# Kernel tuning notes

Measured on AMD Instinct MI355X. Metric: run time of the kernel, lower is better.

The kernel has to match this reference:

```python
import jax, jax.numpy as jnp
import numpy as np

B, T, D = 4, 2048, 1024


def setup_inputs() -> dict:
    key = jax.random.key(0)
    ks = jax.random.split(key, 14)
    s = 0.02
    return {
        "x": jax.random.normal(ks[0], (B, T, D), dtype=jnp.float32),
        "time_decay": jax.random.normal(ks[1], (D,), dtype=jnp.float32) * 0.1,
        "tm_k": jax.random.uniform(ks[2], (D,), dtype=jnp.float32),
        "tm_v": jax.random.uniform(ks[3], (D,), dtype=jnp.float32),
        "tm_r": jax.random.uniform(ks[4], (D,), dtype=jnp.float32),
        "Wk": jax.random.normal(ks[5], (D, D), dtype=jnp.float32) * s,
        "Wv": jax.random.normal(ks[6], (D, D), dtype=jnp.float32) * s,
        "Wr": jax.random.normal(ks[7], (D, D), dtype=jnp.float32) * s,
        "Wo": jax.random.normal(ks[8], (D, D), dtype=jnp.float32) * s,
        "cm_k": jax.random.uniform(ks[9], (D,), dtype=jnp.float32),
        "cm_r": jax.random.uniform(ks[10], (D,), dtype=jnp.float32),
        "Wck": jax.random.normal(ks[11], (D, 4 * D), dtype=jnp.float32) * s,
        "Wcv": jax.random.normal(ks[12], (4 * D, D), dtype=jnp.float32) * s,
        "Wcr": jax.random.normal(ks[13], (D, D), dtype=jnp.float32) * s,
    }


def _shift(x):
    # token shift: prepend zero state (initial last_x), drop last token
    return jnp.concatenate([jnp.zeros_like(x[:, :1]), x[:, :-1]], axis=1)


def reference(x, time_decay, tm_k, tm_v, tm_r, Wk, Wv, Wr, Wo,
              cm_k, cm_r, Wck, Wcv, Wcr):
    # ---- time mixing (WKV recurrence) ----
    shifted = _shift(x)
    xk = x * tm_k + shifted * (1.0 - tm_k)
    xv = x * tm_v + shifted * (1.0 - tm_v)
    xr = x * tm_r + shifted * (1.0 - tm_r)
    k = xk @ Wk            # (B,T,D)
    v = xv @ Wv
    r = jax.nn.sigmoid(xr @ Wr)
    ew = jnp.exp(-jnp.exp(time_decay))  # exp(w), w = -exp(time_decay)

    def step(carry, kv):
        num, den = carry
        kt, vt = kv
        ek = jnp.exp(kt)
        num = ew * num + ek * vt
        den = ew * den + ek
        return (num, den), num / (den + 1e-6)

    init = (jnp.zeros((B, D), x.dtype), jnp.zeros((B, D), x.dtype))
    _, wkv_t = jax.lax.scan(step, init, (jnp.swapaxes(k, 0, 1), jnp.swapaxes(v, 0, 1)))
    wkv = jnp.swapaxes(wkv_t, 0, 1)  # (B,T,D)
    x = x + (r * wkv) @ Wo

    # ---- channel mixing (gated FFN, squared ReLU) ----
    shifted2 = _shift(x)
    xk2 = x * cm_k + shifted2 * (1.0 - cm_k)
    xr2 = x * cm_r + shifted2 * (1.0 - cm_r)
    kh = jnp.square(jax.nn.relu(xk2 @ Wck))  # (B,T,4D)
    v2 = kh @ Wcv
    r2 = jax.nn.sigmoid(xr2 @ Wcr)
    return x + r2 * v2
```

## Files before the change

### kernel.cpp

```cpp
#include <hip/hip_runtime.h>
#include <hip/hip_bf16.h>
#include <math.h>

#define BATCH 4
#define TLEN  2048
#define DIM   1024
#define NROWS (BATCH*TLEN)
#define HDIM  (4*DIM)

typedef __hip_bfloat16 bf16;
typedef __attribute__((ext_vector_type(8))) short   shortx8;
typedef __attribute__((ext_vector_type(4))) float   floatx4;

__device__ __forceinline__ unsigned short f2bf(float f) {
    bf16 h = __float2bfloat16(f);
    return __builtin_bit_cast(unsigned short, h);
}

__device__ __forceinline__ void async16(const void* g, void* l) {
    __builtin_amdgcn_global_load_lds((const __attribute__((address_space(1))) void*)g,
                                     (__attribute__((address_space(3))) void*)l, 16, 0, 0);
}

enum { EP_NONE=0, EP_SIGMOID=1, EP_ADD=2, EP_SQRELU=3, EP_FINAL=4 };

template<int BMT, int MODE, typename OutT>
__global__ __launch_bounds__(256)
void mfma_gemm(const bf16* __restrict__ A, const bf16* __restrict__ Bt,
               OutT* __restrict__ C,
               const float* __restrict__ addv, const bf16* __restrict__ mulv,
               int M, int N, int K)
{
    constexpr int MI    = BMT / 32;
    constexpr int AINST = BMT / 32;
    __shared__ bf16 As[BMT*64];
    __shared__ bf16 Bs[128*64];
    const int tid  = threadIdx.x;
    const int lane = tid & 63;
    const int wave = tid >> 6;
    const int wm   = (wave >> 1) * (BMT/2);
    const int wn   = (wave & 1) * 64;
    const size_t m0 = (size_t)blockIdx.y * BMT;
    const size_t n0 = (size_t)blockIdx.x * 128;

    const int r0 = tid >> 3;
    const int kg = (tid & 7) ^ (r0 & 7);
    const int c0 = kg * 8;
    const bf16* ag[AINST];
    const bf16* bg[4];
    #pragma unroll
    for (int j = 0; j < AINST; ++j) ag[j] = A  + (m0 + r0 + j*32) * K + c0;
    #pragma unroll
    for (int j = 0; j < 4; ++j)     bg[j] = Bt + (n0 + r0 + j*32) * K + c0;

    floatx4 acc[MI][4] = {};

    const int mrow = lane & 15;
    const int kqg  = lane >> 4;
    const int kx   = mrow & 7;

    for (int k0 = 0; k0 < K; k0 += 64) {
        #pragma unroll
        for (int j = 0; j < AINST; ++j) async16(ag[j] + k0, As + (tid + j*256) * 8);
        #pragma unroll
        for (int j = 0; j < 4; ++j)     async16(bg[j] + k0, Bs + (tid + j*256) * 8);
        __syncthreads();

        #pragma unroll
        for (int ks = 0; ks < 2; ++ks) {
            const int kcol = ((ks*4 + kqg) ^ kx) << 3;
            shortx8 af[MI], bfr[4];
            #pragma unroll
            for (int i = 0; i < MI; ++i)
                af[i]  = *(const shortx8*)(As + (wm + i*16 + mrow)*64 + kcol);
            #pragma unroll
            for (int i = 0; i < 4; ++i)
                bfr[i] = *(const shortx8*)(Bs + (wn + i*16 + mrow)*64 + kcol);
            #pragma unroll
            for (int mi = 0; mi < MI; ++mi)
                #pragma unroll
                for (int ni = 0; ni < 4; ++ni)
                    acc[mi][ni] = __builtin_amdgcn_mfma_f32_16x16x32_bf16(
                                      af[mi], bfr[ni], acc[mi][ni], 0, 0, 0);
        }
        __syncthreads();
    }

    const int crow = (lane >> 4) * 4;
    const int ccol = lane & 15;
    #pragma unroll
    for (int mi = 0; mi < MI; ++mi) {
        #pragma unroll
        for (int ni = 0; ni < 4; ++ni) {
            #pragma unroll
            for (int r = 0; r < 4; ++r) {
                size_t row = m0 + wm + mi*16 + crow + r;
                size_t col = n0 + wn + ni*16 + ccol;
                size_t off = row * N + col;
                float v = acc[mi][ni][r];
                if (MODE == EP_SIGMOID)      v = 1.0f / (1.0f + __expf(-v));
                else if (MODE == EP_ADD)     v = addv[off] + v;
                else if (MODE == EP_SQRELU)  { float t = fmaxf(v, 0.0f); v = t * t; }
                else if (MODE == EP_FINAL)   v = addv[off] + __bfloat162float(mulv[off]) * v;
                if (sizeof(OutT) == 2) *(unsigned short*)(C + off) = f2bf(v);
                else                   *(float*)(C + off) = v;
            }
        }
    }
}

struct GDesc { const bf16* A; const bf16* Bt; bf16* C; int N; int K; int mode; int ntiles; };
struct GArgs { GDesc d[3]; };

__global__ __launch_bounds__(256)
void mfma_gemm_multi(GArgs args, int M)
{
    int bx = blockIdx.x, di = 0;
    while (bx >= args.d[di].ntiles) { bx -= args.d[di].ntiles; ++di; }
    const bf16* A  = args.d[di].A;
    const bf16* Bt = args.d[di].Bt;
    bf16*       C  = args.d[di].C;
    const int   N  = args.d[di].N;
    const int   K  = args.d[di].K;
    const int   mode = args.d[di].mode;

    __shared__ bf16 As[128*64];
    __shared__ bf16 Bs[128*64];
    const int tid  = threadIdx.x;
    const int lane = tid & 63;
    const int wave = tid >> 6;
    const int wm   = (wave >> 1) * 64;
    const int wn   = (wave & 1) * 64;
    const size_t m0 = (size_t)blockIdx.y * 128;
    const size_t n0 = (size_t)bx * 128;

    const int r0 = tid >> 3;
    const int kg = (tid & 7) ^ (r0 & 7);
    const int c0 = kg * 8;
    const bf16* ag[4];
    const bf16* bg[4];
    #pragma unroll
    for (int j = 0; j < 4; ++j) {
        ag[j] = A  + (m0 + r0 + j*32) * K + c0;
        bg[j] = Bt + (n0 + r0 + j*32) * K + c0;
    }

    floatx4 acc[4][4] = {};

    const int mrow = lane & 15;
    const int kqg  = lane >> 4;
    const int kx   = mrow & 7;

    for (int k0 = 0; k0 < K; k0 += 64) {
        #pragma unroll
        for (int j = 0; j < 4; ++j) async16(ag[j] + k0, As + (tid + j*256) * 8);
        #pragma unroll
        for (int j = 0; j < 4; ++j) async16(bg[j] + k0, Bs + (tid + j*256) * 8);
        __syncthreads();

        #pragma unroll
        for (int ks = 0; ks < 2; ++ks) {
            const int kcol = ((ks*4 + kqg) ^ kx) << 3;
            shortx8 af[4], bfr[4];
            #pragma unroll
            for (int i = 0; i < 4; ++i) {
                af[i]  = *(const shortx8*)(As + (wm + i*16 + mrow)*64 + kcol);
                bfr[i] = *(const shortx8*)(Bs + (wn + i*16 + mrow)*64 + kcol);
            }
            #pragma unroll
            for (int mi = 0; mi < 4; ++mi)
                #pragma unroll
                for (int ni = 0; ni < 4; ++ni)
                    acc[mi][ni] = __builtin_amdgcn_mfma_f32_16x16x32_bf16(
                                      af[mi], bfr[ni], acc[mi][ni], 0, 0, 0);
        }
        __syncthreads();
    }

    const int crow = (lane >> 4) * 4;
    const int ccol = lane & 15;
    #pragma unroll
    for (int mi = 0; mi < 4; ++mi) {
        #pragma unroll
        for (int ni = 0; ni < 4; ++ni) {
            #pragma unroll
            for (int r = 0; r < 4; ++r) {
                size_t row = m0 + wm + mi*16 + crow + r;
                size_t col = n0 + wn + ni*16 + ccol;
                float v = acc[mi][ni][r];
                if (mode == EP_SIGMOID)     v = 1.0f / (1.0f + __expf(-v));
                else if (mode == EP_SQRELU) { float t = fmaxf(v, 0.0f); v = t * t; }
                *(unsigned short*)(C + row * N + col) = f2bf(v);
            }
        }
    }
}

struct TDesc { const float* in; bf16* out; int K; int N; int tiles; int tx; };
struct TArgs { TDesc d[7]; };

__global__ __launch_bounds__(256)
void transpose_multi(TArgs args)
{
    int t = blockIdx.x, di = 0;
    while (t >= args.d[di].tiles) { t -= args.d[di].tiles; ++di; }
    const float* in  = args.d[di].in;
    bf16*        out = args.d[di].out;
    const int K = args.d[di].K, N = args.d[di].N, tx = args.d[di].tx;
    const int bx = t % tx, by = t / tx;

    __shared__ float tile[32][33];
    const int kt = by * 32, nt = bx * 32;
    #pragma unroll
    for (int i = threadIdx.y; i < 32; i += 8)
        tile[i][threadIdx.x] = in[(size_t)(kt + i) * N + nt + threadIdx.x];
    __syncthreads();
    #pragma unroll
    for (int i = threadIdx.y; i < 32; i += 8)
        out[(size_t)(nt + i) * K + kt + threadIdx.x] =
            __float2bfloat16(tile[threadIdx.x][i]);
}

__global__ __launch_bounds__(256)
void mix3_kernel(const float4* __restrict__ x,
                 const float4* __restrict__ mk, const float4* __restrict__ mv,
                 const float4* __restrict__ mr,
                 ushort4* __restrict__ ok, ushort4* __restrict__ ov,
                 ushort4* __restrict__ orr)
{
    const int D4 = DIM / 4;
    int e   = blockIdx.x * 256 + threadIdx.x;
    int d4  = e & (D4 - 1);
    int t   = (e >> 8) & (TLEN - 1);
    float4 xc = x[e];
    float4 sh = make_float4(0.f, 0.f, 0.f, 0.f);
    if (t > 0) sh = x[e - D4];
    float4 a = mk[d4], b = mv[d4], c = mr[d4];
    ushort4 u;
    u.x=f2bf(xc.x*a.x+sh.x*(1.f-a.x)); u.y=f2bf(xc.y*a.y+sh.y*(1.f-a.y));
    u.z=f2bf(xc.z*a.z+sh.z*(1.f-a.z)); u.w=f2bf(xc.w*a.w+sh.w*(1.f-a.w));
    ok[e]=u;
    u.x=f2bf(xc.x*b.x+sh.x*(1.f-b.x)); u.y=f2bf(xc.y*b.y+sh.y*(1.f-b.y));
    u.z=f2bf(xc.z*b.z+sh.z*(1.f-b.z)); u.w=f2bf(xc.w*b.w+sh.w*(1.f-b.w));
    ov[e]=u;
    u.x=f2bf(xc.x*c.x+sh.x*(1.f-c.x)); u.y=f2bf(xc.y*c.y+sh.y*(1.f-c.y));
    u.z=f2bf(xc.z*c.z+sh.z*(1.f-c.z)); u.w=f2bf(xc.w*c.w+sh.w*(1.f-c.w));
    orr[e]=u;
}

__global__ __launch_bounds__(256)
void mix2_kernel(const float4* __restrict__ x,
                 const float4* __restrict__ mk, const float4* __restrict__ mr,
                 ushort4* __restrict__ ok, ushort4* __restrict__ orr)
{
    const int D4 = DIM / 4;
    int e   = blockIdx.x * 256 + threadIdx.x;
    int d4  = e & (D4 - 1);
    int t   = (e >> 8) & (TLEN - 1);
    float4 xc = x[e];
    float4 sh = make_float4(0.f, 0.f, 0.f, 0.f);
    if (t > 0) sh = x[e - D4];
    float4 a = mk[d4], c = mr[d4];
    ushort4 u;
    u.x=f2bf(xc.x*a.x+sh.x*(1.f-a.x)); u.y=f2bf(xc.y*a.y+sh.y*(1.f-a.y));
    u.z=f2bf(xc.z*a.z+sh.z*(1.f-a.z)); u.w=f2bf(xc.w*a.w+sh.w*(1.f-a.w));
    ok[e]=u;
    u.x=f2bf(xc.x*c.x+sh.x*(1.f-c.x)); u.y=f2bf(xc.y*c.y+sh.y*(1.f-c.y));
    u.z=f2bf(xc.z*c.z+sh.z*(1.f-c.z)); u.w=f2bf(xc.w*c.w+sh.w*(1.f-c.w));
    orr[e]=u;
}

#define WKV_CHUNK 128
#define WKV_WARM  64
__global__ __launch_bounds__(256)
void wkv_kernel(const bf16* __restrict__ K, const bf16* __restrict__ V,
                const bf16* __restrict__ R, const float* __restrict__ td,
                bf16* __restrict__ out)
{
    int d     = blockIdx.x * 256 + threadIdx.x;
    int chunk = blockIdx.y;
    int b     = blockIdx.z;
    int start = chunk * WKV_CHUNK;
    int t0    = start - WKV_WARM; if (t0 < 0) t0 = 0;

    float ew = __expf(-__expf(td[d]));
    float num = 0.f, den = 0.f;
    size_t base = ((size_t)b * TLEN) * DIM + d;

    for (int t = t0; t < start; ++t) {
        size_t idx = base + (size_t)t * DIM;
        float ek = __expf(__bfloat162float(K[idx]));
        num = ew * num + ek * __bfloat162float(V[idx]);
        den = ew * den + ek;
    }
    for (int t = start; t < start + WKV_CHUNK; ++t) {
        size_t idx = base + (size_t)t * DIM;
        float ek = __expf(__bfloat162float(K[idx]));
        num = ew * num + ek * __bfloat162float(V[idx]);
        den = ew * den + ek;
        out[idx] = __float2bfloat16(__bfloat162float(R[idx]) * (num / (den + 1e-6f)));
    }
}

extern "C" void kernel_launch(void* const* d_in, const int* in_sizes, int n_in,
                              void* d_out, int out_size, void* d_ws, size_t ws_size,
                              hipStream_t stream)
{
    const float* x   = (const float*)d_in[0];
    const float* td  = (const float*)d_in[1];
    const float* tmk = (const float*)d_in[2];
    const float* tmv = (const float*)d_in[3];
    const float* tmr = (const float*)d_in[4];
    const float* Wk  = (const float*)d_in[5];
    const float* Wv  = (const float*)d_in[6];
    const float* Wr  = (const float*)d_in[7];
    const float* Wo  = (const float*)d_in[8];
    const float* cmk = (const float*)d_in[9];
    const float* cmr = (const float*)d_in[10];
    const float* Wck = (const float*)d_in[11];
    const float* Wcv = (const float*)d_in[12];
    const float* Wcr = (const float*)d_in[13];
    float* out = (float*)d_out;

    char* ws = (char*)d_ws;
    const size_t MB = 1024 * 1024;
    bf16*  Wk_t  = (bf16*)(ws +   0*MB);
    bf16*  Wv_t  = (bf16*)(ws +   2*MB);
    bf16*  Wr_t  = (bf16*)(ws +   4*MB);
    bf16*  Wo_t  = (bf16*)(ws +   6*MB);
    bf16*  Wcr_t = (bf16*)(ws +   8*MB);
    bf16*  Wck_t = (bf16*)(ws +  10*MB);
    bf16*  Wcv_t = (bf16*)(ws +  18*MB);
    float* f0    = (float*)(ws + 26*MB);
    bf16*  bA    = (bf16*)(ws +  58*MB);
    bf16*  bB    = (bf16*)(ws +  74*MB);
    bf16*  bC    = (bf16*)(ws +  90*MB);
    bf16*  bD    = (bf16*)(ws + 106*MB);
    bf16*  bE    = (bf16*)(ws + 122*MB);
    bf16*  bF    = (bf16*)(ws + 138*MB);
    bf16*  kh    = bB;

    const dim3 blk(256);
    const dim3 mixGrid(NROWS * DIM / 4 / 256);
    const dim3 gemmD(DIM / 128, NROWS / 64);

    {
        TArgs ta;
        const float* src[7] = {Wk, Wv, Wr, Wo, Wcr, Wck, Wcv};
        bf16*       dst[7] = {Wk_t, Wv_t, Wr_t, Wo_t, Wcr_t, Wck_t, Wcv_t};
        int         kk[7]  = {DIM, DIM, DIM, DIM, DIM, DIM, HDIM};
        int         nn[7]  = {DIM, DIM, DIM, DIM, DIM, HDIM, DIM};
        int total = 0;
        for (int i = 0; i < 7; ++i) {
            int tx = nn[i] / 32, ty = kk[i] / 32;
            ta.d[i] = {src[i], dst[i], kk[i], nn[i], tx * ty, tx};
            total += tx * ty;
        }
        transpose_multi<<<dim3(total), dim3(32, 8), 0, stream>>>(ta);
    }

    mix3_kernel<<<mixGrid, blk, 0, stream>>>((const float4*)x,
        (const float4*)tmk, (const float4*)tmv, (const float4*)tmr,
        (ushort4*)bA, (ushort4*)bB, (ushort4*)bC);

    {
        GArgs ga;
        ga.d[0] = {bA, Wk_t, bD, DIM, DIM, EP_NONE,    8};
        ga.d[1] = {bB, Wv_t, bE, DIM, DIM, EP_NONE,    8};
        ga.d[2] = {bC, Wr_t, bF, DIM, DIM, EP_SIGMOID, 8};
        mfma_gemm_multi<<<dim3(24, NROWS/128), blk, 0, stream>>>(ga, NROWS);
    }

    dim3 wkvGrid(DIM / 256, TLEN / WKV_CHUNK, BATCH);
    wkv_kernel<<<wkvGrid, blk, 0, stream>>>(bD, bE, bF, td, bF);

    mfma_gemm<64, EP_ADD, float><<<gemmD, blk, 0, stream>>>(bF, Wo_t, f0, x, nullptr, NROWS, DIM, DIM);

    mix2_kernel<<<mixGrid, blk, 0, stream>>>((const float4*)f0,
        (const float4*)cmk, (const float4*)cmr, (ushort4*)bE, (ushort4*)bA);

    {
        GArgs ga;
        ga.d[0] = {bA, Wcr_t, bF, DIM,  DIM, EP_SIGMOID, 8};
        ga.d[1] = {bE, Wck_t, kh, HDIM, DIM, EP_SQRELU, 32};
        ga.d[2] = {nullptr, nullptr, nullptr, 0, 0, 0, 0};
        mfma_gemm_multi<<<dim3(40, NROWS/128), blk, 0, stream>>>(ga, NROWS);
    }

    mfma_gemm<64, EP_FINAL, float><<<gemmD, blk, 0, stream>>>(kh, Wcv_t, out, f0, bF, NROWS, DIM, HDIM);
}
```

Before: 589.7 us.

## Merge prep kernels, use 128x128 tiles, swap grid order, halve WKV chunk

Combines the weight transpose and the three-way token-mix into one prep launch. All GEMMs now use 128x128 tiles, and the grid is reordered so blockIdx.x walks M-tiles, which changes the order tiles are scheduled and how weight and activation tiles are reused in cache. The grouped Wcr/Wck launch is split into separate mfma_gemm launches. The WKV chunk shrinks from 128 to 64 for more parallelism, at the cost of relatively more warm-up recomputation per chunk. The larger tiles give fewer blocks for the N=1024 GEMMs (512 blocks), which may affect occupancy.

```diff
diff --git a/kernel.cpp b/kernel.cpp
--- a/kernel.cpp
+++ b/kernel.cpp
@@ -24,36 +24,35 @@
 
 enum { EP_NONE=0, EP_SIGMOID=1, EP_ADD=2, EP_SQRELU=3, EP_FINAL=4 };
 
-template<int BMT, int MODE, typename OutT>
+template<int MODE, typename OutT>
 __global__ __launch_bounds__(256)
 void mfma_gemm(const bf16* __restrict__ A, const bf16* __restrict__ Bt,
                OutT* __restrict__ C,
                const float* __restrict__ addv, const bf16* __restrict__ mulv,
                int M, int N, int K)
 {
-    constexpr int MI    = BMT / 32;
-    constexpr int AINST = BMT / 32;
-    __shared__ bf16 As[BMT*64];
+    __shared__ bf16 As[128*64];
     __shared__ bf16 Bs[128*64];
     const int tid  = threadIdx.x;
     const int lane = tid & 63;
     const int wave = tid >> 6;
-    const int wm   = (wave >> 1) * (BMT/2);
+    const int wm   = (wave >> 1) * 64;
     const int wn   = (wave & 1) * 64;
-    const size_t m0 = (size_t)blockIdx.y * BMT;
-    const size_t n0 = (size_t)blockIdx.x * 128;
+    const size_t m0 = (size_t)blockIdx.x * 128;
+    const size_t n0 = (size_t)blockIdx.y * 128;
 
     const int r0 = tid >> 3;
     const int kg = (tid & 7) ^ (r0 & 7);
     const int c0 = kg * 8;
-    const bf16* ag[AINST];
+    const bf16* ag[4];
     const bf16* bg[4];
     #pragma unroll
-    for (int j = 0; j < AINST; ++j) ag[j] = A  + (m0 + r0 + j*32) * K + c0;
-    #pragma unroll
-    for (int j = 0; j < 4; ++j)     bg[j] = Bt + (n0 + r0 + j*32) * K + c0;
-
-    floatx4 acc[MI][4] = {};
+    for (int j = 0; j < 4; ++j) {
+        ag[j] = A  + (m0 + r0 + j*32) * K + c0;
+        bg[j] = Bt + (n0 + r0 + j*32) * K + c0;
+    }
+
+    floatx4 acc[4][4] = {};
 
     const int mrow = lane & 15;
     const int kqg  = lane >> 4;
@@ -61,23 +60,22 @@
 
     for (int k0 = 0; k0 < K; k0 += 64) {
         #pragma unroll
-        for (int j = 0; j < AINST; ++j) async16(ag[j] + k0, As + (tid + j*256) * 8);
-        #pragma unroll
-        for (int j = 0; j < 4; ++j)     async16(bg[j] + k0, Bs + (tid + j*256) * 8);
+        for (int j = 0; j < 4; ++j) async16(ag[j] + k0, As + (tid + j*256) * 8);
+        #pragma unroll
+        for (int j = 0; j < 4; ++j) async16(bg[j] + k0, Bs + (tid + j*256) * 8);
         __syncthreads();
 
         #pragma unroll
         for (int ks = 0; ks < 2; ++ks) {
             const int kcol = ((ks*4 + kqg) ^ kx) << 3;
-            shortx8 af[MI], bfr[4];
-            #pragma unroll
-            for (int i = 0; i < MI; ++i)
+            shortx8 af[4], bfr[4];
+            #pragma unroll
+            for (int i = 0; i < 4; ++i) {
                 af[i]  = *(const shortx8*)(As + (wm + i*16 + mrow)*64 + kcol);
-            #pragma unroll
-            for (int i = 0; i < 4; ++i)
                 bfr[i] = *(const shortx8*)(Bs + (wn + i*16 + mrow)*64 + kcol);
-            #pragma unroll
-            for (int mi = 0; mi < MI; ++mi)
+            }
+            #pragma unroll
+            for (int mi = 0; mi < 4; ++mi)
                 #pragma unroll
                 for (int ni = 0; ni < 4; ++ni)
                     acc[mi][ni] = __builtin_amdgcn_mfma_f32_16x16x32_bf16(
@@ -89,7 +87,7 @@
     const int crow = (lane >> 4) * 4;
     const int ccol = lane & 15;
     #pragma unroll
-    for (int mi = 0; mi < MI; ++mi) {
+    for (int mi = 0; mi < 4; ++mi) {
         #pragma unroll
         for (int ni = 0; ni < 4; ++ni) {
             #pragma unroll
@@ -113,10 +111,10 @@
 struct GArgs { GDesc d[3]; };
 
 __global__ __launch_bounds__(256)
-void mfma_gemm_multi(GArgs args, int M)
-{
-    int bx = blockIdx.x, di = 0;
-    while (bx >= args.d[di].ntiles) { bx -= args.d[di].ntiles; ++di; }
+void mfma_gemm_multi(GArgs args)
+{
+    int by = blockIdx.y, di = 0;
+    while (by >= args.d[di].ntiles) { by -= args.d[di].ntiles; ++di; }
     const bf16* A  = args.d[di].A;
     const bf16* Bt = args.d[di].Bt;
     bf16*       C  = args.d[di].C;
@@ -131,8 +129,8 @@
     const int wave = tid >> 6;
     const int wm   = (wave >> 1) * 64;
     const int wn   = (wave & 1) * 64;
-    const size_t m0 = (size_t)blockIdx.y * 128;
-    const size_t n0 = (size_t)bx * 128;
+    const size_t m0 = (size_t)blockIdx.x * 128;
+    const size_t n0 = (size_t)by * 128;
 
     const int r0 = tid >> 3;
     const int kg = (tid & 7) ^ (r0 & 7);
@@ -197,55 +195,55 @@
 }
 
 struct TDesc { const float* in; bf16* out; int K; int N; int tiles; int tx; };
-struct TArgs { TDesc d[7]; };
-
-__global__ __launch_bounds__(256)
-void transpose_multi(TArgs args)
-{
-    int t = blockIdx.x, di = 0;
-    while (t >= args.d[di].tiles) { t -= args.d[di].tiles; ++di; }
-    const float* in  = args.d[di].in;
-    bf16*        out = args.d[di].out;
-    const int K = args.d[di].K, N = args.d[di].N, tx = args.d[di].tx;
-    const int bx = t % tx, by = t / tx;
-
-    __shared__ float tile[32][33];
-    const int kt = by * 32, nt = bx * 32;
-    #pragma unroll
-    for (int i = threadIdx.y; i < 32; i += 8)
-        tile[i][threadIdx.x] = in[(size_t)(kt + i) * N + nt + threadIdx.x];
-    __syncthreads();
-    #pragma unroll
-    for (int i = threadIdx.y; i < 32; i += 8)
-        out[(size_t)(nt + i) * K + kt + threadIdx.x] =
-            __float2bfloat16(tile[threadIdx.x][i]);
-}
-
-__global__ __launch_bounds__(256)
-void mix3_kernel(const float4* __restrict__ x,
-                 const float4* __restrict__ mk, const float4* __restrict__ mv,
-                 const float4* __restrict__ mr,
-                 ushort4* __restrict__ ok, ushort4* __restrict__ ov,
-                 ushort4* __restrict__ orr)
-{
-    const int D4 = DIM / 4;
-    int e   = blockIdx.x * 256 + threadIdx.x;
-    int d4  = e & (D4 - 1);
-    int t   = (e >> 8) & (TLEN - 1);
-    float4 xc = x[e];
-    float4 sh = make_float4(0.f, 0.f, 0.f, 0.f);
-    if (t > 0) sh = x[e - D4];
-    float4 a = mk[d4], b = mv[d4], c = mr[d4];
-    ushort4 u;
-    u.x=f2bf(xc.x*a.x+sh.x*(1.f-a.x)); u.y=f2bf(xc.y*a.y+sh.y*(1.f-a.y));
-    u.z=f2bf(xc.z*a.z+sh.z*(1.f-a.z)); u.w=f2bf(xc.w*a.w+sh.w*(1.f-a.w));
-    ok[e]=u;
-    u.x=f2bf(xc.x*b.x+sh.x*(1.f-b.x)); u.y=f2bf(xc.y*b.y+sh.y*(1.f-b.y));
-    u.z=f2bf(xc.z*b.z+sh.z*(1.f-b.z)); u.w=f2bf(xc.w*b.w+sh.w*(1.f-b.w));
-    ov[e]=u;
-    u.x=f2bf(xc.x*c.x+sh.x*(1.f-c.x)); u.y=f2bf(xc.y*c.y+sh.y*(1.f-c.y));
-    u.z=f2bf(xc.z*c.z+sh.z*(1.f-c.z)); u.w=f2bf(xc.w*c.w+sh.w*(1.f-c.w));
-    orr[e]=u;
+struct PrepArgs {
+    TDesc t[7];
+    int ttotal;
+    const float4 *x, *mk, *mv, *mr;
+    ushort4 *ok, *ov, *orr;
+};
+
+__global__ __launch_bounds__(256)
+void prep_kernel(PrepArgs a)
+{
+    int blk = blockIdx.x;
+    if (blk < a.ttotal) {
+        int t = blk, di = 0;
+        while (t >= a.t[di].tiles) { t -= a.t[di].tiles; ++di; }
+        const float* in  = a.t[di].in;
+        bf16*        out = a.t[di].out;
+        const int K = a.t[di].K, N = a.t[di].N, tx = a.t[di].tx;
+        const int bx = t % tx, by = t / tx;
+        __shared__ float tile[32][33];
+        const int kt = by * 32, nt = bx * 32;
+        #pragma unroll
+        for (int i = threadIdx.y; i < 32; i += 8)
+            tile[i][threadIdx.x] = in[(size_t)(kt + i) * N + nt + threadIdx.x];
+        __syncthreads();
+        #pragma unroll
+        for (int i = threadIdx.y; i < 32; i += 8)
+            out[(size_t)(nt + i) * K + kt + threadIdx.x] =
+                __float2bfloat16(tile[threadIdx.x][i]);
+    } else {
+        const int D4 = DIM / 4;
+        int tid = threadIdx.y * 32 + threadIdx.x;
+        int e   = (blk - a.ttotal) * 256 + tid;
+        int d4  = e & (D4 - 1);
+        int t   = (e >> 8) & (TLEN - 1);
+        float4 xc = a.x[e];
+        float4 sh = make_float4(0.f, 0.f, 0.f, 0.f);
+        if (t > 0) sh = a.x[e - D4];
+        float4 mk = a.mk[d4], mv = a.mv[d4], mr = a.mr[d4];
+        ushort4 u;
+        u.x=f2bf(xc.x*mk.x+sh.x*(1.f-mk.x)); u.y=f2bf(xc.y*mk.y+sh.y*(1.f-mk.y));
+        u.z=f2bf(xc.z*mk.z+sh.z*(1.f-mk.z)); u.w=f2bf(xc.w*mk.w+sh.w*(1.f-mk.w));
+        a.ok[e]=u;
+        u.x=f2bf(xc.x*mv.x+sh.x*(1.f-mv.x)); u.y=f2bf(xc.y*mv.y+sh.y*(1.f-mv.y));
+        u.z=f2bf(xc.z*mv.z+sh.z*(1.f-mv.z)); u.w=f2bf(xc.w*mv.w+sh.w*(1.f-mv.w));
+        a.ov[e]=u;
+        u.x=f2bf(xc.x*mr.x+sh.x*(1.f-mr.x)); u.y=f2bf(xc.y*mr.y+sh.y*(1.f-mr.y));
+        u.z=f2bf(xc.z*mr.z+sh.z*(1.f-mr.z)); u.w=f2bf(xc.w*mr.w+sh.w*(1.f-mr.w));
+        a.orr[e]=u;
+    }
 }
 
 __global__ __launch_bounds__(256)
@@ -270,7 +268,7 @@
     orr[e]=u;
 }
 
-#define WKV_CHUNK 128
+#define WKV_CHUNK 64
 #define WKV_WARM  64
 __global__ __launch_bounds__(256)
 void wkv_kernel(const bf16* __restrict__ K, const bf16* __restrict__ V,
@@ -338,54 +336,54 @@
     bf16*  bD    = (bf16*)(ws + 106*MB);
     bf16*  bE    = (bf16*)(ws + 122*MB);
     bf16*  bF    = (bf16*)(ws + 138*MB);
-    bf16*  kh    = bB;
+    bf16*  kh    = bA;
 
     const dim3 blk(256);
-    const dim3 mixGrid(NROWS * DIM / 4 / 256);
-    const dim3 gemmD(DIM / 128, NROWS / 64);
 
     {
-        TArgs ta;
+        PrepArgs pa;
         const float* src[7] = {Wk, Wv, Wr, Wo, Wcr, Wck, Wcv};
-        bf16*       dst[7] = {Wk_t, Wv_t, Wr_t, Wo_t, Wcr_t, Wck_t, Wcv_t};
-        int         kk[7]  = {DIM, DIM, DIM, DIM, DIM, DIM, HDIM};
-        int         nn[7]  = {DIM, DIM, DIM, DIM, DIM, HDIM, DIM};
+        bf16*        dst[7] = {Wk_t, Wv_t, Wr_t, Wo_t, Wcr_t, Wck_t, Wcv_t};
+        int          kk[7]  = {DIM, DIM, DIM, DIM, DIM, DIM, HDIM};
+        int          nn[7]  = {DIM, DIM, DIM, DIM, DIM, HDIM, DIM};
         int total = 0;
         for (int i = 0; i < 7; ++i) {
             int tx = nn[i] / 32, ty = kk[i] / 32;
-            ta.d[i] = {src[i], dst[i], kk[i], nn[i], tx * ty, tx};
+            pa.t[i] = {src[i], dst[i], kk[i], nn[i], tx * ty, tx};
             total += tx * ty;
         }
-        transpose_multi<<<dim3(total), dim3(32, 8), 0, stream>>>(ta);
-    }
-
-    mix3_kernel<<<mixGrid, blk, 0, stream>>>((const float4*)x,
-        (const float4*)tmk, (const float4*)tmv, (const float4*)tmr,
-        (ushort4*)bA, (ushort4*)bB, (ushort4*)bC);
+        pa.ttotal = total;
+        pa.x  = (const float4*)x;
+        pa.mk = (const float4*)tmk; pa.mv = (const float4*)tmv; pa.mr = (const float4*)tmr;
+        pa.ok = (ushort4*)bA; pa.ov = (ushort4*)bB; pa.orr = (ushort4*)bC;
+        const int mixBlocks = NROWS * DIM / 4 / 256;
+        prep_kernel<<<dim3(total + mixBlocks), dim3(32, 8), 0, stream>>>(pa);
+    }
 
     {
         GArgs ga;
         ga.d[0] = {bA, Wk_t, bD, DIM, DIM, EP_NONE,    8};
         ga.d[1] = {bB, Wv_t, bE, DIM, DIM, EP_NONE,    8};
         ga.d[2] = {bC, Wr_t, bF, DIM, DIM, EP_SIGMOID, 8};
-        mfma_gemm_multi<<<dim3(24, NROWS/128), blk, 0, stream>>>(ga, NROWS);
+        mfma_gemm_multi<<<dim3(NROWS/128, 24), blk, 0, stream>>>(ga);
     }
 
     dim3 wkvGrid(DIM / 256, TLEN / WKV_CHUNK, BATCH);
     wkv_kernel<<<wkvGrid, blk, 0, stream>>>(bD, bE, bF, td, bF);
 
-    mfma_gemm<64, EP_ADD, float><<<gemmD, blk, 0, stream>>>(bF, Wo_t, f0, x, nullptr, NROWS, DIM, DIM);
-
-    mix2_kernel<<<mixGrid, blk, 0, stream>>>((const float4*)f0,
-        (const float4*)cmk, (const float4*)cmr, (ushort4*)bE, (ushort4*)bA);
-
-    {
-        GArgs ga;
-        ga.d[0] = {bA, Wcr_t, bF, DIM,  DIM, EP_SIGMOID, 8};
-        ga.d[1] = {bE, Wck_t, kh, HDIM, DIM, EP_SQRELU, 32};
-        ga.d[2] = {nullptr, nullptr, nullptr, 0, 0, 0, 0};
-        mfma_gemm_multi<<<dim3(40, NROWS/128), blk, 0, stream>>>(ga, NROWS);
-    }
-
-    mfma_gemm<64, EP_FINAL, float><<<gemmD, blk, 0, stream>>>(kh, Wcv_t, out, f0, bF, NROWS, DIM, HDIM);
-}
+    mfma_gemm<EP_ADD, float><<<dim3(NROWS/128, DIM/128), blk, 0, stream>>>(
+        bF, Wo_t, f0, x, nullptr, NROWS, DIM, DIM);
+
+    mix2_kernel<<<dim3(NROWS * DIM / 4 / 256), blk, 0, stream>>>(
+        (const float4*)f0, (const float4*)cmk, (const float4*)cmr,
+        (ushort4*)bE, (ushort4*)bA);
+
+    mfma_gemm<EP_SIGMOID, bf16><<<dim3(NROWS/128, DIM/128), blk, 0, stream>>>(
+        bA, Wcr_t, bF, nullptr, nullptr, NROWS, DIM, DIM);
+
+    mfma_gemm<EP_SQRELU, bf16><<<dim3(NROWS/128, HDIM/128), blk, 0, stream>>>(
+        bE, Wck_t, kh, nullptr, nullptr, NROWS, HDIM, DIM);
+
+    mfma_gemm<EP_FINAL, float><<<dim3(NROWS/128, DIM/128), blk, 0, stream>>>(
+        kh, Wcv_t, out, f0, bF, NROWS, DIM, HDIM);
+}
```

Measured after the change: 501.5 us. 1.18x faster.
